# Kernel tuning notes

Measured on AMD Instinct MI355X. Metric: run time of the kernel, lower is better.

## Reference

```python
import jax, jax.numpy as jnp
import numpy as np

SCORE_THRESHOLD = 0.3
IOU_THRESHOLD = 0.5
MAX_DETECTIONS = 100
NEG_INF = -jnp.inf
B, N, C = 8, 16384, 80


def setup_inputs() -> dict:
    key = jax.random.key(0)
    kb, ks = jax.random.split(key)
    raw = jax.random.uniform(kb, (B, N, 4), dtype=jnp.float32)
    ymin = raw[..., 0] * 0.8
    xmin = raw[..., 1] * 0.8
    ymax = ymin + 0.02 + raw[..., 2] * 0.2
    xmax = xmin + 0.02 + raw[..., 3] * 0.2
    boxes = jnp.stack([ymin, xmin, ymax, xmax], axis=-1)  # valid corner boxes
    scores = jax.random.uniform(ks, (B, N, C), dtype=jnp.float32)
    return {"boxes": boxes, "scores": scores}


def _iou_one_vs_all(sel, boxes, areas):
    # sel: [B,C,4] currently-selected box per class; boxes: [B,N,4]; areas: [B,N] -> iou [B,C,N]
    b = sel[:, :, None, :]      # [B,C,1,4]
    o = boxes[:, None, :, :]    # [B,1,N,4]
    yy1 = jnp.maximum(b[..., 0], o[..., 0])
    xx1 = jnp.maximum(b[..., 1], o[..., 1])
    yy2 = jnp.minimum(b[..., 2], o[..., 2])
    xx2 = jnp.minimum(b[..., 3], o[..., 3])
    inter = jnp.maximum(yy2 - yy1, 0.0) * jnp.maximum(xx2 - xx1, 0.0)
    area_sel = jnp.maximum(sel[..., 2] - sel[..., 0], 0.0) * jnp.maximum(sel[..., 3] - sel[..., 1], 0.0)  # [B,C]
    union = area_sel[..., None] + areas[:, None, :] - inter
    return inter / jnp.maximum(union, 1e-9)


def multiclass_nms(boxes, scores):
    # boxes [B,N,4], scores [B,N,C]
    s0 = jnp.where(scores > SCORE_THRESHOLD, scores, NEG_INF).transpose(0, 2, 1)  # [B,C,N]
    areas = jnp.maximum(boxes[..., 2] - boxes[..., 0], 0.0) * jnp.maximum(boxes[..., 3] - boxes[..., 1], 0.0)  # [B,N]
    bidx = jnp.arange(B)[:, None]

    def step(s, _):
        idx = jnp.argmax(s, axis=-1)                                    # [B,C]
        sc = jnp.take_along_axis(s, idx[..., None], axis=-1)[..., 0]    # [B,C]
        kept = jnp.isfinite(sc)                                         # valid pick?
        sel = boxes[bidx, idx]                                          # [B,C,4]
        iou = _iou_one_vs_all(sel, boxes, areas)                        # [B,C,N]
        onehot = jax.nn.one_hot(idx, N, dtype=bool)
        supp = kept[..., None] & ((iou >= IOU_THRESHOLD) | onehot)
        s_new = jnp.where(supp, NEG_INF, s)
        out_sc = jnp.where(kept, sc, 0.0)
        out_box = jnp.where(kept[..., None], sel, 0.0)
        return s_new, (out_box, out_sc, kept)

    _, (db, ds, dk) = jax.lax.scan(step, s0, None, length=MAX_DETECTIONS)
    # db [T,B,C,4], ds [T,B,C], dk [T,B,C] -> flatten class/time -> [B, C*T]
    T = MAX_DETECTIONS
    db = jnp.transpose(db, (1, 2, 0, 3)).reshape(B, C * T, 4)
    ds = jnp.transpose(ds, (1, 2, 0)).reshape(B, C * T)
    dk = jnp.transpose(dk, (1, 2, 0)).reshape(B, C * T)
    labels = jnp.broadcast_to(jnp.repeat(jnp.arange(C), T)[None, :], (B, C * T))

    masked = jnp.where(dk, ds, NEG_INF)
    _, top_idx = jax.lax.top_k(masked, MAX_DETECTIONS)                  # merge classes, descending scores
    top_sc = jnp.take_along_axis(ds, top_idx, axis=1)
    top_valid = jnp.take_along_axis(dk, top_idx, axis=1)
    top_boxes = jnp.take_along_axis(db, top_idx[..., None], axis=1)
    top_labels = jnp.take_along_axis(labels, top_idx, axis=1)

    out_boxes = jnp.where(top_valid[..., None], top_boxes, 0.0)
    out_scores = jnp.where(top_valid, top_sc, 0.0)
    out_labels = jnp.where(top_valid, top_labels, 0).astype(jnp.int32)
    valid_detections = top_valid.sum(axis=1).astype(jnp.int32)
    return out_boxes, out_scores, out_labels, valid_detections


def reference(boxes, scores):
    return jax.jit(multiclass_nms)(boxes, scores)
```

## Files before the change

kernel.cpp:

```cpp
#include <hip/hip_runtime.h>
#include <math.h>
#include <stdint.h>

#define BB 8
#define NN 16384
#define CC 80
#define TT 100
#define CAP 1024
#define BAND_LO 0.984375f
#define BASEBITS 0x3F7C0000u
#define LCAP 24
#define SLICES 64
#define ROWS 256

typedef unsigned int u32;
typedef unsigned long long u64;

__device__ __forceinline__ void bitonic_desc32(u32* buf, int n2, int tid) {
  for (int k = 2; k <= n2; k <<= 1)
    for (int j = k >> 1; j > 0; j >>= 1) {
      for (int i = tid; i < n2; i += 256) {
        int ixj = i ^ j;
        if (ixj > i) {
          u32 a = buf[i], d2 = buf[ixj];
          bool up = ((i & k) == 0);
          if (up ? (a < d2) : (a > d2)) { buf[i] = d2; buf[ixj] = a; }
        }
      }
      __syncthreads();
    }
}
__device__ __forceinline__ void bitonic_desc64(u64* buf, int n2, int tid) {
  for (int k = 2; k <= n2; k <<= 1)
    for (int j = k >> 1; j > 0; j >>= 1) {
      for (int i = tid; i < n2; i += 256) {
        int ixj = i ^ j;
        if (ixj > i) {
          u64 a = buf[i], d2 = buf[ixj];
          bool up = ((i & k) == 0);
          if (up ? (a < d2) : (a > d2)) { buf[i] = d2; buf[ixj] = a; }
        }
      }
      __syncthreads();
    }
}

__global__ __launch_bounds__(256) void gather_kernel(const float* __restrict__ scores,
                                                     u32* __restrict__ cand,
                                                     int* __restrict__ cnts) {
  __shared__ u32 lkeys[CC * LCAP];
  __shared__ int lcnt[CC];

  int b = blockIdx.x / SLICES;
  int slice = blockIdx.x % SLICES;
  int n0 = slice * ROWS;
  int tid = threadIdx.x;

  if (tid < CC) lcnt[tid] = 0;
  __syncthreads();

  const float4* s4 = (const float4*)scores;
  size_t base4 = ((size_t)b * NN + n0) * (CC / 4);
  for (int i = tid; i < ROWS * (CC / 4); i += 256) {
    float4 q = s4[base4 + i];
    int ib = i * 4;
    float vv[4] = {q.x, q.y, q.z, q.w};
#pragma unroll
    for (int e = 0; e < 4; ++e) {
      float v = vv[e];
      if (v >= BAND_LO) {
        int fe = ib + e;
        int c = fe % CC;
        int n = n0 + fe / CC;
        int s = atomicAdd(&lcnt[c], 1);
        if (s < LCAP)
          lkeys[c * LCAP + s] = ((__float_as_uint(v) - BASEBITS) << 14) | (u32)(16383 - n);
      }
    }
  }
  __syncthreads();

  int bc0 = b * CC;
  if (tid < CC) cnts[(size_t)(bc0 + tid) * SLICES + slice] = lcnt[tid];
  for (int idx = tid; idx < CC * LCAP; idx += 256) {
    int c = idx / LCAP, i = idx % LCAP;
    int lc = lcnt[c]; if (lc > LCAP) lc = LCAP;
    if (i < lc) cand[((size_t)(bc0 + c) * SLICES + slice) * LCAP + i] = lkeys[idx];
  }
}

__global__ __launch_bounds__(256) void nms_kernel(const float* __restrict__ boxes,
                                                  const float* __restrict__ scores,
                                                  const u32* __restrict__ cand,
                                                  const int* __restrict__ cnts,
                                                  float* __restrict__ det_score,
                                                  float* __restrict__ det_box) {
  __shared__ u64 keys[CAP];
  __shared__ float sv[CAP];
  __shared__ float4 bxs[CAP];
  __shared__ float4 abx[TT];
  __shared__ float aarea[TT];
  __shared__ u32 killp[4][64];
  __shared__ int partial[256];
  __shared__ int off_s[SLICES], x_s[SLICES];
  __shared__ int mtot_s, ok_s, nacc_s, cnt_s;

  int bc = blockIdx.x;
  int b = bc / CC, c = bc % CC;
  int tid = threadIdx.x;
  const float* bsrc = boxes + (size_t)b * NN * 4;
  float* dsc = det_score + (size_t)bc * TT;
  float4* dbx = (float4*)det_box + (size_t)bc * TT;
  u32* k32 = (u32*)keys;

  if (tid < 64) {
    int craw = cnts[(size_t)bc * SLICES + tid];
    int okl = (craw <= LCAP) ? 1 : 0;
    bool ok = __all(okl);
    int x = (craw > LCAP) ? LCAP : craw;
    int incl = x;
#pragma unroll
    for (int d = 1; d < 64; d <<= 1) {
      int y = __shfl_up(incl, d);
      if (tid >= d) incl += y;
    }
    off_s[tid] = incl - x; x_s[tid] = x;
    if (tid == 63) mtot_s = incl;
    if (tid == 0) { ok_s = ok ? 1 : 0; nacc_s = 0; }
  }
  __syncthreads();
  int m_total = mtot_s;
  bool pre_ok = ok_s && (m_total <= CAP);
  if (pre_ok) {
    int slice = tid >> 2, li = tid & 3;
    int x = x_s[slice], off = off_s[slice];
    const u32* seg = cand + ((size_t)bc * SLICES + slice) * LCAP;
    for (int i = li; i < x; i += 4) k32[off + i] = seg[i];
  }
  __syncthreads();

  float lo = BAND_LO, hi = INFINITY;
  bool first = true;
  int nacc = 0;

  for (;;) {
    int m;
    bool fast = first && pre_ok;
    if (fast) {
      m = m_total;
      if (m > 0) {
        int n2 = 64; while (n2 < m) n2 <<= 1;
        for (int s = m + tid; s < n2; s += 256) k32[s] = 0u;
        __syncthreads();
        bitonic_desc32(k32, n2, tid);
        for (int s = tid; s < m; s += 256) {
          u32 k = k32[s];
          sv[s] = __uint_as_float(BASEBITS + (k >> 14));
          u32 n = 16383u - (k & 16383u);
          bxs[s] = *(const float4*)(bsrc + (size_t)n * 4);
        }
        __syncthreads();
      }
    } else {
      float band_lo = lo;
      for (int tries = 0;; ++tries) {
        if (tid == 0) cnt_s = 0;
        __syncthreads();
        for (int n = tid; n < NN; n += 256) {
          float v = scores[((size_t)b * NN + n) * CC + c];
          if (v > 0.3f && v >= band_lo && v < hi) {
            int s = atomicAdd(&cnt_s, 1);
            if (s < CAP) keys[s] = ((u64)__float_as_uint(v) << 32) | (u32)(~(u32)n);
          }
        }
        __syncthreads();
        if (cnt_s <= CAP || tries >= 24) break;
        float hi_eff = (hi > 1.0f) ? 1.0f : hi;
        band_lo = 0.5f * (band_lo + hi_eff);
        __syncthreads();
      }
      m = (cnt_s < CAP) ? cnt_s : CAP;
      lo = band_lo;
      if (m > 0) {
        int n2 = 64; while (n2 < m) n2 <<= 1;
        for (int s = m + tid; s < n2; s += 256) keys[s] = 0ull;
        __syncthreads();
        bitonic_desc64(keys, n2, tid);
        for (int s = tid; s < m; s += 256) {
          u64 k = keys[s];
          sv[s] = __uint_as_float((u32)(k >> 32));
          u32 n = ~(u32)k;
          bxs[s] = *(const float4*)(bsrc + (size_t)n * 4);
        }
        __syncthreads();
      }
    }
    first = false;

    if (m > 0) {
      int nchunks = (m + 63) >> 6;
      int j = tid & 63, blk = tid >> 6;
      for (int ch = 0; ch < nchunks; ++ch) {
        int na = nacc_s;
        if (na >= TT) break;
        int sj = ch * 64 + j;
        bool have = sj < m;
        float4 bj = have ? bxs[sj] : make_float4(0.f, 0.f, 0.f, 0.f);
        float aj = fmaxf(bj.z - bj.x, 0.f) * fmaxf(bj.w - bj.y, 0.f);

        int dead = have ? 0 : 1;
        for (int a = blk; a < na; a += 4) {
          float4 ab = abx[a]; float aa = aarea[a];
          float yy1 = fmaxf(ab.x, bj.x), xx1 = fmaxf(ab.y, bj.y);
          float yy2 = fminf(ab.z, bj.z), xx2 = fminf(ab.w, bj.w);
          float inter = fmaxf(yy2 - yy1, 0.f) * fmaxf(xx2 - xx1, 0.f);
          float uni = aa + aj - inter;
          if (inter / fmaxf(uni, 1e-9f) >= 0.5f) dead = 1;
        }
        partial[tid] = dead;

        u32 kp = 0;
#pragma unroll
        for (int r = 0; r < 16; ++r) {
          int i = blk * 16 + r;
          float4 bi = bxs[ch * 64 + i];
          float ai = fmaxf(bi.z - bi.x, 0.f) * fmaxf(bi.w - bi.y, 0.f);
          float yy1 = fmaxf(bj.x, bi.x), xx1 = fmaxf(bj.y, bi.y);
          float yy2 = fminf(bj.z, bi.z), xx2 = fminf(bj.w, bi.w);
          float inter = fmaxf(yy2 - yy1, 0.f) * fmaxf(xx2 - xx1, 0.f);
          float uni = aj + ai - inter;
          if (i > j && (inter / fmaxf(uni, 1e-9f) >= 0.5f)) kp |= (1u << r);
        }
        killp[blk][j] = kp;
        __syncthreads();

        if (tid < 64) {
          int l = tid;
          int d0 = partial[l] | partial[64 + l] | partial[128 + l] | partial[192 + l];
          u32 klo = killp[0][l] | (killp[1][l] << 16);
          u32 khi = killp[2][l] | (killp[3][l] << 16);
          u64 deadm = __ballot(d0 != 0);
          u64 accb = 0ull;
          int space = TT - na;
          for (int jj = 0; jj < 64; ++jj) {
            if (!((deadm >> jj) & 1ull)) {
              accb |= (1ull << jj);
              if ((int)__popcll(accb) >= space) break;
              u64 kj = ((u64)(u32)__shfl((int)klo, jj)) |
                       (((u64)(u32)__shfl((int)khi, jj)) << 32);
              deadm |= kj;
            }
          }
          bool accme = ((accb >> l) & 1ull) != 0;
          if (accme) {
            int rank = __popcll(accb & ((1ull << l) - 1ull));
            int slot = na + rank;
            abx[slot] = bj; aarea[slot] = aj;
            dsc[slot] = sv[ch * 64 + l];
            dbx[slot] = bj;
          }
          if (l == 0) nacc_s = na + (int)__popcll(accb);
        }
        __syncthreads();
      }
    }

    nacc = nacc_s;
    if (nacc >= TT || lo <= 0.0f) break;
    hi = lo;
    float nlo = lo - 0.03f;
    lo = (nlo <= 0.31f) ? 0.0f : nlo;
    __syncthreads();
  }
  for (int t = nacc + tid; t < TT; t += 256) dsc[t] = -INFINITY;
}

__global__ __launch_bounds__(256) void topk_select(const float* __restrict__ det_score,
                                                   const float* __restrict__ det_box,
                                                   float* __restrict__ out) {
  __shared__ u64 kk[CC * TT];
  __shared__ u64 buf[8192];
  __shared__ int scnt[CC];
  __shared__ int total_s, base_s, vc_s;

  int b = blockIdx.x, tid = threadIdx.x;
  for (int i = tid; i < CC * TT; i += 256) {
    float v = det_score[(size_t)b * CC * TT + i];
    kk[i] = (v == -INFINITY) ? 0ull : (((u64)__float_as_uint(v) << 32) | (u32)(~(u32)i));
  }
  if (tid == 0) { total_s = 0; base_s = 0; vc_s = 0; }
  __syncthreads();

  for (int i = tid; i < 256; i += 256) buf[i] = (i < 2 * CC) ? kk[(i >> 1) * TT + (i & 1)] : 0ull;
  __syncthreads();
  bitonic_desc64(buf, 256, tid);
  u64 t = buf[99];
  u64 tq = t ? t : 1ull;
  __syncthreads();

  if (tid < CC) {
    int lo2 = 0, hi2 = TT;
    while (lo2 < hi2) {
      int mid = (lo2 + hi2) >> 1;
      if (kk[tid * TT + mid] >= tq) lo2 = mid + 1; else hi2 = mid;
    }
    scnt[tid] = lo2;
    atomicAdd(&total_s, lo2);
  }
  __syncthreads();
  int total = total_s;
  int n2 = 128;
  while (n2 < total) n2 <<= 1;

  if (tid < CC) {
    int m = scnt[tid];
    int gb = atomicAdd(&base_s, m);
    for (int i = 0; i < m; ++i) buf[gb + i] = kk[tid * TT + i];
  }
  __syncthreads();
  for (int i = total + tid; i < n2; i += 256) buf[i] = 0ull;
  __syncthreads();
  bitonic_desc64(buf, n2, tid);

  float* ob = out + (size_t)b * TT * 4;
  float* os = out + BB * TT * 4 + (size_t)b * TT;
  float* ol = out + BB * TT * 5 + (size_t)b * TT;
  if (tid < TT) {
    u64 k = buf[tid];
    bool valid = (k != 0ull);
    u32 j = valid ? (u32)(~(u32)k) : 0u;
    float v = __uint_as_float((u32)(k >> 32));
    float4 bx = make_float4(0.f, 0.f, 0.f, 0.f);
    if (valid) bx = *(const float4*)(det_box + ((size_t)b * CC * TT + j) * 4);
    ((float4*)ob)[tid] = bx;
    os[tid] = valid ? v : 0.0f;
    ol[tid] = valid ? (float)(j / TT) : 0.0f;
    if (valid) atomicAdd(&vc_s, 1);
  }
  __syncthreads();
  if (tid == 0) out[BB * TT * 5 + BB * TT + b] = (float)vc_s;
}

extern "C" void kernel_launch(void* const* d_in, const int* in_sizes, int n_in,
                              void* d_out, int out_size, void* d_ws, size_t ws_size,
                              hipStream_t stream) {
  const float* boxes  = (const float*)d_in[0];
  const float* scores = (const float*)d_in[1];
  float* out = (float*)d_out;

  char* ws = (char*)d_ws;
  const size_t CAND_B = (size_t)BB * CC * SLICES * LCAP * 4;
  const size_t CNTS_B = (size_t)BB * CC * SLICES * 4;
  const size_t DBX_B  = (size_t)BB * CC * TT * 16;
  u32*   cand      = (u32*)ws;
  int*   cnts      = (int*)(ws + CAND_B);
  float* det_box   = (float*)(ws + CAND_B + CNTS_B);
  float* det_score = (float*)(ws + CAND_B + CNTS_B + DBX_B);

  gather_kernel<<<BB * SLICES, 256, 0, stream>>>(scores, cand, cnts);
  nms_kernel<<<BB * CC, 256, 0, stream>>>(boxes, scores, cand, cnts, det_score, det_box);
  topk_select<<<BB, 256, 0, stream>>>(det_score, det_box, out);
}
```

Before: 154.7 us.

## Precompute IoU suppression bitmask for fast path and use register bitonic sorts

Narrows the fast-path score band and caps candidates at 256. The fast path now sorts with a register/shuffle-based bitonic network and builds a pairwise IoU suppression bitmask matrix in parallel, so greedy selection becomes a single-thread bit-scan instead of chunked IoU checks against accepted boxes. The top-k merge kernel also switches to the hybrid register sort for 256-element sorts. The risk is that the narrower band yields fewer than 100 detections more often, which would trigger the slow rescanning fallback. The serial single-thread greedy loop is another possible bottleneck.

```diff
diff --git a/kernel.cpp b/kernel.cpp
--- a/kernel.cpp
+++ b/kernel.cpp
@@ -7,8 +7,9 @@
 #define CC 80
 #define TT 100
 #define CAP 1024
-#define BAND_LO 0.984375f
-#define BASEBITS 0x3F7C0000u
+#define MMAX 256
+#define BAND_LO 0.98828125f
+#define BASEBITS 0x3F7D0000u
 #define LCAP 24
 #define SLICES 64
 #define ROWS 256
@@ -16,20 +17,12 @@
 typedef unsigned int u32;
 typedef unsigned long long u64;
 
-__device__ __forceinline__ void bitonic_desc32(u32* buf, int n2, int tid) {
-  for (int k = 2; k <= n2; k <<= 1)
-    for (int j = k >> 1; j > 0; j >>= 1) {
-      for (int i = tid; i < n2; i += 256) {
-        int ixj = i ^ j;
-        if (ixj > i) {
-          u32 a = buf[i], d2 = buf[ixj];
-          bool up = ((i & k) == 0);
-          if (up ? (a < d2) : (a > d2)) { buf[i] = d2; buf[ixj] = a; }
-        }
-      }
-      __syncthreads();
-    }
-}
+__device__ __forceinline__ u64 shfl_xor_u64(u64 v, int m) {
+  int lo = __shfl_xor((int)(u32)v, m);
+  int hi = __shfl_xor((int)(v >> 32), m);
+  return ((u64)(u32)hi << 32) | (u32)lo;
+}
+
 __device__ __forceinline__ void bitonic_desc64(u64* buf, int n2, int tid) {
   for (int k = 2; k <= n2; k <<= 1)
     for (int j = k >> 1; j > 0; j >>= 1) {
@@ -43,6 +36,34 @@
       }
       __syncthreads();
     }
+}
+
+__device__ __forceinline__ void hybrid_sort256_u64(u64* buf, int tid) {
+  u64 r = buf[tid];
+  for (int k = 2; k <= 256; k <<= 1)
+    for (int j = k >> 1; j > 0; j >>= 1) {
+      int keep_max = (((tid & k) == 0) == ((tid & j) == 0));
+      u64 other;
+      if (j >= 64) { __syncthreads(); buf[tid] = r; __syncthreads(); other = buf[tid ^ j]; }
+      else other = shfl_xor_u64(r, j);
+      u64 mx = (r > other) ? r : other, mn = (r > other) ? other : r;
+      r = keep_max ? mx : mn;
+    }
+  __syncthreads(); buf[tid] = r; __syncthreads();
+}
+
+__device__ __forceinline__ void hybrid_sort256_u32(u32* buf, int tid) {
+  u32 r = buf[tid];
+  for (int k = 2; k <= 256; k <<= 1)
+    for (int j = k >> 1; j > 0; j >>= 1) {
+      int keep_max = (((tid & k) == 0) == ((tid & j) == 0));
+      u32 other;
+      if (j >= 64) { __syncthreads(); buf[tid] = r; __syncthreads(); other = buf[tid ^ j]; }
+      else other = __shfl_xor(r, j);
+      u32 mx = (r > other) ? r : other, mn = (r > other) ? other : r;
+      r = keep_max ? mx : mn;
+    }
+  __syncthreads(); buf[tid] = r; __syncthreads();
 }
 
 __global__ __launch_bounds__(256) void gather_kernel(const float* __restrict__ scores,
@@ -98,8 +119,10 @@
   __shared__ u64 keys[CAP];
   __shared__ float sv[CAP];
   __shared__ float4 bxs[CAP];
+  __shared__ u64 kcol[MMAX * 4];
   __shared__ float4 abx[TT];
   __shared__ float aarea[TT];
+  __shared__ int order_s[TT];
   __shared__ u32 killp[4][64];
   __shared__ int partial[256];
   __shared__ int off_s[SLICES], x_s[SLICES];
@@ -130,7 +153,7 @@
   }
   __syncthreads();
   int m_total = mtot_s;
-  bool pre_ok = ok_s && (m_total <= CAP);
+  bool pre_ok = ok_s && (m_total <= MMAX);
   if (pre_ok) {
     int slice = tid >> 2, li = tid & 3;
     int x = x_s[slice], off = off_s[slice];
@@ -139,65 +162,119 @@
   }
   __syncthreads();
 
-  float lo = BAND_LO, hi = INFINITY;
-  bool first = true;
   int nacc = 0;
-
-  for (;;) {
+  float lo, hi;
+
+  if (pre_ok) {
+    int m = m_total;
+    for (int s = m + tid; s < MMAX; s += 256) k32[s] = 0u;
+    __syncthreads();
+    hybrid_sort256_u32(k32, tid);
+    if (tid < m) {
+      u32 k = k32[tid];
+      sv[tid] = __uint_as_float(BASEBITS + (k >> 14));
+      u32 n = 16383u - (k & 16383u);
+      bxs[tid] = *(const float4*)(bsrc + (size_t)n * 4);
+    }
+    __syncthreads();
+    if (tid < m) {
+      float4 bj = bxs[tid];
+      float aj = fmaxf(bj.z - bj.x, 0.f) * fmaxf(bj.w - bj.y, 0.f);
+#pragma unroll
+      for (int w = 0; w < 4; ++w) {
+        u64 kw = 0ull;
+        int i0 = w << 6, i1 = (m < i0 + 64) ? m : (i0 + 64);
+        for (int i = i0; i < i1; ++i) {
+          float4 bi = bxs[i];
+          float ai = fmaxf(bi.z - bi.x, 0.f) * fmaxf(bi.w - bi.y, 0.f);
+          float yy1 = fmaxf(bj.x, bi.x), xx1 = fmaxf(bj.y, bi.y);
+          float yy2 = fminf(bj.z, bi.z), xx2 = fminf(bj.w, bi.w);
+          float inter = fmaxf(yy2 - yy1, 0.f) * fmaxf(xx2 - xx1, 0.f);
+          float uni = aj + ai - inter;
+          if (i != tid && (inter / fmaxf(uni, 1e-9f) >= 0.5f)) kw |= (1ull << (i - i0));
+        }
+        kcol[tid * 4 + w] = kw;
+      }
+    }
+    __syncthreads();
+    if (tid == 0) {
+      u64 live[4];
+#pragma unroll
+      for (int w = 0; w < 4; ++w) {
+        int lo_i = w << 6;
+        live[w] = (m <= lo_i) ? 0ull : ((m >= lo_i + 64) ? ~0ull : ((1ull << (m - lo_i)) - 1ull));
+      }
+      int na = 0;
+      while (na < TT) {
+        int j;
+        if (live[0]) j = __ffsll(live[0]) - 1;
+        else if (live[1]) j = 64 + __ffsll(live[1]) - 1;
+        else if (live[2]) j = 128 + __ffsll(live[2]) - 1;
+        else if (live[3]) j = 192 + __ffsll(live[3]) - 1;
+        else break;
+        live[j >> 6] &= ~(1ull << (j & 63));
+        order_s[na++] = j;
+        const u64* kc = &kcol[(size_t)j * 4];
+        live[0] &= ~kc[0]; live[1] &= ~kc[1]; live[2] &= ~kc[2]; live[3] &= ~kc[3];
+      }
+      nacc_s = na;
+    }
+    __syncthreads();
+    nacc = nacc_s;
+    if (tid < nacc) {
+      int j = order_s[tid];
+      float4 bj = bxs[j];
+      dsc[tid] = sv[j];
+      dbx[tid] = bj;
+      abx[tid] = bj;
+      aarea[tid] = fmaxf(bj.z - bj.x, 0.f) * fmaxf(bj.w - bj.y, 0.f);
+    }
+    __syncthreads();
+    lo = BAND_LO - 0.03f; if (lo <= 0.31f) lo = 0.0f;
+    hi = BAND_LO;
+  } else {
+    lo = BAND_LO;
+    hi = INFINITY;
+  }
+
+  while (nacc < TT && !(pre_ok && hi == BAND_LO && nacc >= TT)) {
+    if (pre_ok && nacc >= TT) break;
+    if (nacc >= TT) break;
+    if (pre_ok && lo > hi) break;
+    float band_lo = lo;
     int m;
-    bool fast = first && pre_ok;
-    if (fast) {
-      m = m_total;
-      if (m > 0) {
-        int n2 = 64; while (n2 < m) n2 <<= 1;
-        for (int s = m + tid; s < n2; s += 256) k32[s] = 0u;
-        __syncthreads();
-        bitonic_desc32(k32, n2, tid);
-        for (int s = tid; s < m; s += 256) {
-          u32 k = k32[s];
-          sv[s] = __uint_as_float(BASEBITS + (k >> 14));
-          u32 n = 16383u - (k & 16383u);
-          bxs[s] = *(const float4*)(bsrc + (size_t)n * 4);
-        }
-        __syncthreads();
-      }
-    } else {
-      float band_lo = lo;
-      for (int tries = 0;; ++tries) {
-        if (tid == 0) cnt_s = 0;
-        __syncthreads();
-        for (int n = tid; n < NN; n += 256) {
-          float v = scores[((size_t)b * NN + n) * CC + c];
-          if (v > 0.3f && v >= band_lo && v < hi) {
-            int s = atomicAdd(&cnt_s, 1);
-            if (s < CAP) keys[s] = ((u64)__float_as_uint(v) << 32) | (u32)(~(u32)n);
-          }
-        }
-        __syncthreads();
-        if (cnt_s <= CAP || tries >= 24) break;
-        float hi_eff = (hi > 1.0f) ? 1.0f : hi;
-        band_lo = 0.5f * (band_lo + hi_eff);
-        __syncthreads();
-      }
-      m = (cnt_s < CAP) ? cnt_s : CAP;
-      lo = band_lo;
-      if (m > 0) {
-        int n2 = 64; while (n2 < m) n2 <<= 1;
-        for (int s = m + tid; s < n2; s += 256) keys[s] = 0ull;
-        __syncthreads();
-        bitonic_desc64(keys, n2, tid);
-        for (int s = tid; s < m; s += 256) {
-          u64 k = keys[s];
-          sv[s] = __uint_as_float((u32)(k >> 32));
-          u32 n = ~(u32)k;
-          bxs[s] = *(const float4*)(bsrc + (size_t)n * 4);
-        }
-        __syncthreads();
-      }
-    }
-    first = false;
+    for (int tries = 0;; ++tries) {
+      if (tid == 0) cnt_s = 0;
+      __syncthreads();
+      for (int n = tid; n < NN; n += 256) {
+        float v = scores[((size_t)b * NN + n) * CC + c];
+        if (v > 0.3f && v >= band_lo && v < hi) {
+          int s = atomicAdd(&cnt_s, 1);
+          if (s < CAP) keys[s] = ((u64)__float_as_uint(v) << 32) | (u32)(~(u32)n);
+        }
+      }
+      __syncthreads();
+      if (cnt_s <= CAP || tries >= 24) break;
+      float hi_eff = (hi > 1.0f) ? 1.0f : hi;
+      band_lo = 0.5f * (band_lo + hi_eff);
+      __syncthreads();
+    }
+    m = (cnt_s < CAP) ? cnt_s : CAP;
+    lo = band_lo;
 
     if (m > 0) {
+      int n2 = 64; while (n2 < m) n2 <<= 1;
+      for (int s = m + tid; s < n2; s += 256) keys[s] = 0ull;
+      __syncthreads();
+      bitonic_desc64(keys, n2, tid);
+      for (int s = tid; s < m; s += 256) {
+        u64 k = keys[s];
+        sv[s] = __uint_as_float((u32)(k >> 32));
+        u32 n = ~(u32)k;
+        bxs[s] = *(const float4*)(bsrc + (size_t)n * 4);
+      }
+      __syncthreads();
+
       int nchunks = (m + 63) >> 6;
       int j = tid & 63, blk = tid >> 6;
       for (int ch = 0; ch < nchunks; ++ch) {
@@ -272,6 +349,7 @@
     lo = (nlo <= 0.31f) ? 0.0f : nlo;
     __syncthreads();
   }
+
   for (int t = nacc + tid; t < TT; t += 256) dsc[t] = -INFINITY;
 }
 
@@ -291,9 +369,9 @@
   if (tid == 0) { total_s = 0; base_s = 0; vc_s = 0; }
   __syncthreads();
 
-  for (int i = tid; i < 256; i += 256) buf[i] = (i < 2 * CC) ? kk[(i >> 1) * TT + (i & 1)] : 0ull;
-  __syncthreads();
-  bitonic_desc64(buf, 256, tid);
+  buf[tid] = (tid < 2 * CC) ? kk[(tid >> 1) * TT + (tid & 1)] : 0ull;
+  __syncthreads();
+  hybrid_sort256_u64(buf, tid);
   u64 t = buf[99];
   u64 tq = t ? t : 1ull;
   __syncthreads();
@@ -309,7 +387,7 @@
   }
   __syncthreads();
   int total = total_s;
-  int n2 = 128;
+  int n2 = 256;
   while (n2 < total) n2 <<= 1;
 
   if (tid < CC) {
@@ -320,7 +398,8 @@
   __syncthreads();
   for (int i = total + tid; i < n2; i += 256) buf[i] = 0ull;
   __syncthreads();
-  bitonic_desc64(buf, n2, tid);
+  if (n2 == 256) hybrid_sort256_u64(buf, tid);
+  else bitonic_desc64(buf, n2, tid);
 
   float* ob = out + (size_t)b * TT * 4;
   float* os = out + BB * TT * 4 + (size_t)b * TT;
```

Result: slower. 175.0 us (+13.1%).

## Use shuffle-based 256-wide bitonic sort, narrow the score band, cache box areas

Applied to the files above, without the earlier changes.

Replaces the shared-memory bitonic sorts with a register-resident 256-element sort. Strides below 64 are exchanged with wave shuffles, so the block only synchronises for the wider strides. The pre-gathered score band is narrowed so the per-class candidate count fits in 256, and the fast path is restricted to that size. Box areas are also computed once into shared memory instead of being recomputed inside the IoU loops. The risk is that the narrower band more often leaves fewer than 100 survivors, forcing the slow full-scan fallback.

```diff
diff --git a/kernel.cpp b/kernel.cpp
--- a/kernel.cpp
+++ b/kernel.cpp
@@ -7,8 +7,9 @@
 #define CC 80
 #define TT 100
 #define CAP 1024
-#define BAND_LO 0.984375f
-#define BASEBITS 0x3F7C0000u
+#define MMAX 256
+#define BAND_LO 0.98828125f
+#define BASEBITS 0x3F7D0000u
 #define LCAP 24
 #define SLICES 64
 #define ROWS 256
@@ -16,20 +17,12 @@
 typedef unsigned int u32;
 typedef unsigned long long u64;
 
-__device__ __forceinline__ void bitonic_desc32(u32* buf, int n2, int tid) {
-  for (int k = 2; k <= n2; k <<= 1)
-    for (int j = k >> 1; j > 0; j >>= 1) {
-      for (int i = tid; i < n2; i += 256) {
-        int ixj = i ^ j;
-        if (ixj > i) {
-          u32 a = buf[i], d2 = buf[ixj];
-          bool up = ((i & k) == 0);
-          if (up ? (a < d2) : (a > d2)) { buf[i] = d2; buf[ixj] = a; }
-        }
-      }
-      __syncthreads();
-    }
-}
+__device__ __forceinline__ u64 shfl_xor_u64(u64 v, int m) {
+  int lo = __shfl_xor((int)(u32)v, m);
+  int hi = __shfl_xor((int)(v >> 32), m);
+  return ((u64)(u32)hi << 32) | (u32)lo;
+}
+
 __device__ __forceinline__ void bitonic_desc64(u64* buf, int n2, int tid) {
   for (int k = 2; k <= n2; k <<= 1)
     for (int j = k >> 1; j > 0; j >>= 1) {
@@ -43,6 +36,34 @@
       }
       __syncthreads();
     }
+}
+
+__device__ __forceinline__ void hybrid_sort256_u64(u64* buf, int tid) {
+  u64 r = buf[tid];
+  for (int k = 2; k <= 256; k <<= 1)
+    for (int j = k >> 1; j > 0; j >>= 1) {
+      int keep_max = (((tid & k) == 0) == ((tid & j) == 0));
+      u64 other;
+      if (j >= 64) { __syncthreads(); buf[tid] = r; __syncthreads(); other = buf[tid ^ j]; }
+      else other = shfl_xor_u64(r, j);
+      u64 mx = (r > other) ? r : other, mn = (r > other) ? other : r;
+      r = keep_max ? mx : mn;
+    }
+  __syncthreads(); buf[tid] = r; __syncthreads();
+}
+
+__device__ __forceinline__ void hybrid_sort256_u32(u32* buf, int tid) {
+  u32 r = buf[tid];
+  for (int k = 2; k <= 256; k <<= 1)
+    for (int j = k >> 1; j > 0; j >>= 1) {
+      int keep_max = (((tid & k) == 0) == ((tid & j) == 0));
+      u32 other;
+      if (j >= 64) { __syncthreads(); buf[tid] = r; __syncthreads(); other = buf[tid ^ j]; }
+      else other = __shfl_xor(r, j);
+      u32 mx = (r > other) ? r : other, mn = (r > other) ? other : r;
+      r = keep_max ? mx : mn;
+    }
+  __syncthreads(); buf[tid] = r; __syncthreads();
 }
 
 __global__ __launch_bounds__(256) void gather_kernel(const float* __restrict__ scores,
@@ -98,6 +119,7 @@
   __shared__ u64 keys[CAP];
   __shared__ float sv[CAP];
   __shared__ float4 bxs[CAP];
+  __shared__ float car[CAP];
   __shared__ float4 abx[TT];
   __shared__ float aarea[TT];
   __shared__ u32 killp[4][64];
@@ -130,7 +152,7 @@
   }
   __syncthreads();
   int m_total = mtot_s;
-  bool pre_ok = ok_s && (m_total <= CAP);
+  bool pre_ok = ok_s && (m_total <= MMAX);
   if (pre_ok) {
     int slice = tid >> 2, li = tid & 3;
     int x = x_s[slice], off = off_s[slice];
@@ -148,19 +170,18 @@
     bool fast = first && pre_ok;
     if (fast) {
       m = m_total;
-      if (m > 0) {
-        int n2 = 64; while (n2 < m) n2 <<= 1;
-        for (int s = m + tid; s < n2; s += 256) k32[s] = 0u;
-        __syncthreads();
-        bitonic_desc32(k32, n2, tid);
-        for (int s = tid; s < m; s += 256) {
-          u32 k = k32[s];
-          sv[s] = __uint_as_float(BASEBITS + (k >> 14));
-          u32 n = 16383u - (k & 16383u);
-          bxs[s] = *(const float4*)(bsrc + (size_t)n * 4);
-        }
-        __syncthreads();
-      }
+      for (int s = m + tid; s < MMAX; s += 256) k32[s] = 0u;
+      __syncthreads();
+      hybrid_sort256_u32(k32, tid);
+      if (tid < m) {
+        u32 k = k32[tid];
+        sv[tid] = __uint_as_float(BASEBITS + (k >> 14));
+        u32 n = 16383u - (k & 16383u);
+        float4 bx = *(const float4*)(bsrc + (size_t)n * 4);
+        bxs[tid] = bx;
+        car[tid] = fmaxf(bx.z - bx.x, 0.f) * fmaxf(bx.w - bx.y, 0.f);
+      }
+      __syncthreads();
     } else {
       float band_lo = lo;
       for (int tries = 0;; ++tries) {
@@ -190,7 +211,9 @@
           u64 k = keys[s];
           sv[s] = __uint_as_float((u32)(k >> 32));
           u32 n = ~(u32)k;
-          bxs[s] = *(const float4*)(bsrc + (size_t)n * 4);
+          float4 bx = *(const float4*)(bsrc + (size_t)n * 4);
+          bxs[s] = bx;
+          car[s] = fmaxf(bx.z - bx.x, 0.f) * fmaxf(bx.w - bx.y, 0.f);
         }
         __syncthreads();
       }
@@ -206,7 +229,7 @@
         int sj = ch * 64 + j;
         bool have = sj < m;
         float4 bj = have ? bxs[sj] : make_float4(0.f, 0.f, 0.f, 0.f);
-        float aj = fmaxf(bj.z - bj.x, 0.f) * fmaxf(bj.w - bj.y, 0.f);
+        float aj = have ? car[sj] : 0.f;
 
         int dead = have ? 0 : 1;
         for (int a = blk; a < na; a += 4) {
@@ -224,7 +247,7 @@
         for (int r = 0; r < 16; ++r) {
           int i = blk * 16 + r;
           float4 bi = bxs[ch * 64 + i];
-          float ai = fmaxf(bi.z - bi.x, 0.f) * fmaxf(bi.w - bi.y, 0.f);
+          float ai = car[ch * 64 + i];
           float yy1 = fmaxf(bj.x, bi.x), xx1 = fmaxf(bj.y, bi.y);
           float yy2 = fminf(bj.z, bi.z), xx2 = fminf(bj.w, bi.w);
           float inter = fmaxf(yy2 - yy1, 0.f) * fmaxf(xx2 - xx1, 0.f);
@@ -291,9 +314,9 @@
   if (tid == 0) { total_s = 0; base_s = 0; vc_s = 0; }
   __syncthreads();
 
-  for (int i = tid; i < 256; i += 256) buf[i] = (i < 2 * CC) ? kk[(i >> 1) * TT + (i & 1)] : 0ull;
-  __syncthreads();
-  bitonic_desc64(buf, 256, tid);
+  buf[tid] = (tid < 2 * CC) ? kk[(tid >> 1) * TT + (tid & 1)] : 0ull;
+  __syncthreads();
+  hybrid_sort256_u64(buf, tid);
   u64 t = buf[99];
   u64 tq = t ? t : 1ull;
   __syncthreads();
@@ -309,7 +332,7 @@
   }
   __syncthreads();
   int total = total_s;
-  int n2 = 128;
+  int n2 = 256;
   while (n2 < total) n2 <<= 1;
 
   if (tid < CC) {
@@ -320,7 +343,8 @@
   __syncthreads();
   for (int i = total + tid; i < n2; i += 256) buf[i] = 0ull;
   __syncthreads();
-  bitonic_desc64(buf, n2, tid);
+  if (n2 == 256) hybrid_sort256_u64(buf, tid);
+  else bitonic_desc64(buf, n2, tid);
 
   float* ob = out + (size_t)b * TT * 4;
   float* os = out + BB * TT * 4 + (size_t)b * TT;
```

New measurement: 133.5 us. -13.7%, faster.
